# Kernel tuning notes

Hardware: AMD Instinct MI355X
Metric: run time of the kernel (lower is better)

## Reference

```python
import jax, jax.numpy as jnp
import numpy as np
import math

F_DIM = 512
N_HEADS = 8
HEAD_DIM = F_DIM // N_HEADS
IMG = 16            # image_size
L = IMG ** 3        # voxel sequence length = 4096
PATCH = 196         # patch_number (ViT 14x14)
VIT_RES = 14
RES = 224           # VIEW_IMAGE_RES
SKETCH_DIM = 768
SIGMA = 1.5         # fixed kernel_size (torch draws randomly when None)
GN_GROUPS = 32


def position_encoding(d_model, length):
    pe = np.zeros((length, d_model), dtype=np.float32)
    position = np.arange(length, dtype=np.float32)[:, None]
    div_term = np.exp(np.arange(0, d_model, 2, dtype=np.float32) * -(math.log(10000.0) / d_model))
    pe[:, 0::2] = np.sin(position * div_term)
    pe[:, 1::2] = np.cos(position * div_term)
    return jnp.asarray(pe)


def get_voxel_coordinates(resolution, size=1.0):
    # centers of a resolution^3 grid spanning [-size/2, size/2]
    idx = np.arange(resolution, dtype=np.float32)
    g = np.stack(np.meshgrid(idx, idx, idx, indexing='ij'), -1).reshape(-1, 3)
    return (g + 0.5) / resolution * size - size / 2.0


VOXEL_PE = position_encoding(F_DIM, L)          # (L, F)
COND_PE = position_encoding(F_DIM, PATCH)       # (S, F)
VOXEL_PTS = jnp.asarray(get_voxel_coordinates(IMG))  # (L, 3)
_vg = np.arange(VIT_RES, dtype=np.float32)
VIT_PIXELS = jnp.asarray(np.stack(np.meshgrid(_vg, _vg, indexing='ij'), -1).reshape(PATCH, 2))  # (S, 2)


def setup_inputs() -> dict:
    key = jax.random.key(0)
    ks = jax.random.split(key, 12)
    B = 8
    s = 0.02
    return {
        'x': jax.random.normal(ks[0], (B, F_DIM, IMG, IMG, IMG), jnp.float32),
        'sketch_feature': jax.random.normal(ks[1], (B, PATCH, SKETCH_DIM), jnp.float32),
        'projection_matrix': jax.random.normal(ks[2], (B, 1, 3, 3), jnp.float32),
        'gn_scale': jnp.ones((F_DIM,), jnp.float32),
        'gn_bias': jnp.zeros((F_DIM,), jnp.float32),
        'conv_w': jax.random.normal(ks[3], (F_DIM, F_DIM, 3, 3, 3), jnp.float32) * s,
        'conv_b': jnp.zeros((F_DIM,), jnp.float32),
        'k_w': jax.random.normal(ks[4], (F_DIM, SKETCH_DIM), jnp.float32) * s,
        'k_b': jnp.zeros((F_DIM,), jnp.float32),
        'v_w': jax.random.normal(ks[5], (F_DIM, SKETCH_DIM), jnp.float32) * s,
        'v_b': jnp.zeros((F_DIM,), jnp.float32),
        'in_proj_w': jax.random.normal(ks[6], (3 * F_DIM, F_DIM), jnp.float32) * s,
        'in_proj_b': jnp.zeros((3 * F_DIM,), jnp.float32),
        'out_w': jax.random.normal(ks[7], (F_DIM, F_DIM), jnp.float32) * s,
        'out_b': jnp.zeros((F_DIM,), jnp.float32),
    }


def _group_norm(x, scale, bias, groups=GN_GROUPS, eps=1e-5):
    B, C = x.shape[0], x.shape[1]
    xr = x.reshape(B, groups, C // groups, -1)
    m = xr.mean(axis=(2, 3), keepdims=True)
    v = xr.var(axis=(2, 3), keepdims=True)
    xn = ((xr - m) / jnp.sqrt(v + eps)).reshape(x.shape)
    shp = (1, C) + (1,) * (x.ndim - 2)
    return xn * scale.reshape(shp) + bias.reshape(shp)


def _attn_mask(projection_matrix):
    # project voxel centers, clamp to pixel grid, threshold cdist to vit patch centers
    P = projection_matrix[:, 0]                                  # (B,3,3)
    pc = jnp.einsum('bij,nj->bni', P, VOXEL_PTS)                 # (B,L,3)
    pixels = pc[..., 0:2] / pc[..., 2:3]
    pixels = jnp.clip(jnp.round(pixels), 0.0, RES - 1.0)         # clamp_pixel
    x_idx = (2.0 * pixels[..., 1:2] + 1.0) / RES * VIT_RES / 2.0
    y_idx = (2.0 * (RES - 1.0 - pixels[..., 0:1]) + 1.0) / RES * VIT_RES / 2.0
    ps = jnp.concatenate([x_idx, y_idx], -1) - 0.5               # (B,L,2)
    dist = jnp.linalg.norm(ps[:, :, None, :] - VIT_PIXELS[None, None], axis=-1)  # (B,L,S)
    return jnp.abs(dist) > (SIGMA - 1e-6)                        # True = masked out


def _forward(x, sketch_feature, projection_matrix, gn_scale, gn_bias, conv_w, conv_b,
             k_w, k_b, v_w, v_b, in_proj_w, in_proj_b, out_w, out_b):
    B = x.shape[0]
    # q path: GroupNorm -> SiLU -> Conv3d(3, pad 1)
    h = jax.nn.silu(_group_norm(x, gn_scale, gn_bias))
    h = jax.lax.conv_general_dilated(h, conv_w, window_strides=(1, 1, 1),
                                     padding=[(1, 1)] * 3,
                                     dimension_numbers=('NCDHW', 'OIDHW', 'NCDHW'))
    h = h + conv_b.reshape(1, F_DIM, 1, 1, 1)
    q = h.reshape(B, F_DIM, L).transpose(0, 2, 1) + VOXEL_PE[None]        # (B,L,F)

    mask = _attn_mask(projection_matrix)                                   # (B,L,S)

    k = sketch_feature @ k_w.T + k_b + COND_PE[None]                       # (B,S,F)
    v = sketch_feature @ v_w.T + v_b + COND_PE[None]

    # nn.MultiheadAttention (eval: no dropout)
    wq, wk, wv = jnp.split(in_proj_w, 3, axis=0)
    bq, bk, bv = jnp.split(in_proj_b, 3, axis=0)
    qh = (q @ wq.T + bq).reshape(B, L, N_HEADS, HEAD_DIM).transpose(0, 2, 1, 3)
    kh = (k @ wk.T + bk).reshape(B, PATCH, N_HEADS, HEAD_DIM).transpose(0, 2, 1, 3)
    vh = (v @ wv.T + bv).reshape(B, PATCH, N_HEADS, HEAD_DIM).transpose(0, 2, 1, 3)

    scores = jnp.einsum('bhld,bhsd->bhls', qh, kh) / math.sqrt(HEAD_DIM)   # (B,H,L,S)
    scores = jnp.where(mask[:, None], -jnp.inf, scores)                    # mask shared over heads
    attn = jax.nn.softmax(scores, axis=-1)
    o = jnp.einsum('bhls,bhsd->bhld', attn, vh)
    o = o.transpose(0, 2, 1, 3).reshape(B, L, F_DIM)
    o = o @ out_w.T + out_b                                                # (B,L,F)
    return o.transpose(0, 2, 1).reshape(B, F_DIM, IMG, IMG, IMG)


def reference(x, sketch_feature, projection_matrix, gn_scale, gn_bias, conv_w, conv_b,
              k_w, k_b, v_w, v_b, in_proj_w, in_proj_b, out_w, out_b):
    return _forward(x, sketch_feature, projection_matrix, gn_scale, gn_bias, conv_w, conv_b,
                    k_w, k_b, v_w, v_b, in_proj_w, in_proj_b, out_w, out_b)
```

## Files before the change

kernel.cpp:

```cpp
#include <hip/hip_runtime.h>

#define DEV static __device__ __forceinline__

typedef unsigned short u16;
typedef unsigned int u32;
typedef unsigned long long u64;
typedef float f32x4 __attribute__((ext_vector_type(4)));
typedef short bfrag __attribute__((ext_vector_type(8)));

#define FD 512
#define LV 4096
#define PV 5832

DEV float b2f(u16 u){ union{ u32 i; float f; } x; x.i = ((u32)u)<<16; return x.f; }
DEV u16 f2b(float f){ union{ float f; u32 i; } x; x.f = f; u32 r = x.i; r += 0x7fffu + ((r>>16)&1u); return (u16)(r>>16); }

DEV void g2l(const void* g, void* s){
  __builtin_amdgcn_global_load_lds((const __attribute__((address_space(1))) void*)g,
                                   (__attribute__((address_space(3))) void*)s, 16, 0, 0);
}

static const size_t o_wt  = 0;
static const size_t o_wq  = 14155776;
static const size_t o_ow  = 14680064;
static const size_t o_vpe = 15204352;
static const size_t o_cpe = 23592960;
static const size_t o_gn  = 23994368;
static const size_t o_mask= 23996416;
static const size_t o_khb = 25044992;
static const size_t o_vhb = 26748928;
static const size_t o_hp  = 36841472;
static const size_t o_qb  = 84617216;
static const size_t o_qh  = 118171648;
static const size_t o_skb = o_qh;
static const size_t o_kwb = o_qh + 2555904;
static const size_t o_vwb = o_qh + 3342336;
static const size_t o_wkb = o_qh + 4128768;
static const size_t o_wvb = o_qh + 4653056;
static const size_t o_ktb = o_qh + 5177344;
static const size_t o_vtb = o_qh + 6881280;

__global__ __launch_bounds__(256) void prep_all(const float* __restrict__ convw,
    const float* __restrict__ ipw, const float* __restrict__ ow,
    const float* __restrict__ sketch, const float* __restrict__ kw, const float* __restrict__ vw,
    u16* __restrict__ wt, u16* __restrict__ Wq, u16* __restrict__ Ow, u16* __restrict__ Skb,
    u16* __restrict__ Kwb, u16* __restrict__ Vwb, u16* __restrict__ Wkb, u16* __restrict__ Wvb){
  __shared__ float raw[6912];
  int blk = blockIdx.x, t = threadIdx.x;
  if (blk < 1024){
    size_t base = (size_t)blk*6912;
    #pragma unroll
    for (int j=0;j<27;j++) raw[j*256 + t] = convw[base + j*256 + t];
    __syncthreads();
    int rowb = blk*256;
    #pragma unroll
    for (int k=0;k<27;k++) wt[(size_t)k*262144 + rowb + t] = f2b(raw[t*27 + k]);
  } else if (blk < 2048){ int i=(blk-1024)*256+t;  Wq[i]  = f2b(ipw[i]); }
  else if (blk < 3072){   int i=(blk-2048)*256+t;  Ow[i]  = f2b(ow[i]); }
  else if (blk < 7776){   int i=(blk-3072)*256+t;  if (i<1204224) Skb[i] = f2b(sketch[i]); }
  else if (blk < 9312){   int i=(blk-7776)*256+t;  Kwb[i] = f2b(kw[i]); }
  else if (blk < 10848){  int i=(blk-9312)*256+t;  Vwb[i] = f2b(vw[i]); }
  else if (blk < 11872){  int i=(blk-10848)*256+t; Wkb[i] = f2b(ipw[262144+i]); }
  else {                  int i=(blk-11872)*256+t; Wvb[i] = f2b(ipw[524288+i]); }
}

__global__ __launch_bounds__(256) void geom_prep(float* __restrict__ vpe, float* __restrict__ cpe,
    const float* __restrict__ proj, u64* __restrict__ maskb){
  int blk = blockIdx.x, t = threadIdx.x;
  if (blk < 4292){
    float* pe = (blk < 4096) ? vpe : cpe;
    int l = (blk < 4096) ? blk : blk - 4096;
    const float fac = -0.017988946039015984f;
    float dt = expf((float)(2*t) * fac);
    float ang = (float)l * dt;
    pe[(size_t)l*FD + 2*t]     = sinf(ang);
    pe[(size_t)l*FD + 2*t + 1] = cosf(ang);
    return;
  }
  int idx = (blk-4292)*256 + t;
  int b = idx >> 12, v = idx & 4095;
  float P[9];
  #pragma unroll
  for (int j=0;j<9;j++) P[j] = proj[b*9 + j];
  int zi=v>>8, yi=(v>>4)&15, xi=v&15;
  float pt0 = ((float)zi + 0.5f)/16.0f - 0.5f;
  float pt1 = ((float)yi + 0.5f)/16.0f - 0.5f;
  float pt2 = ((float)xi + 0.5f)/16.0f - 0.5f;
  float pc0 = __fadd_rn(__fadd_rn(__fmul_rn(P[0],pt0), __fmul_rn(P[1],pt1)), __fmul_rn(P[2],pt2));
  float pc1 = __fadd_rn(__fadd_rn(__fmul_rn(P[3],pt0), __fmul_rn(P[4],pt1)), __fmul_rn(P[5],pt2));
  float pc2 = __fadd_rn(__fadd_rn(__fmul_rn(P[6],pt0), __fmul_rn(P[7],pt1)), __fmul_rn(P[8],pt2));
  float r0 = __fdiv_rn(pc0, pc2);
  float r1 = __fdiv_rn(pc1, pc2);
  float px0 = fminf(fmaxf(rintf(r0), 0.f), 223.f);
  float px1 = fminf(fmaxf(rintf(r1), 0.f), 223.f);
  float x_idx = __fmul_rn(__fdiv_rn(__fadd_rn(__fmul_rn(2.f,px1),1.f), 224.f), 14.f) * 0.5f;
  float y_idx = __fmul_rn(__fdiv_rn(__fadd_rn(__fmul_rn(2.f,__fadd_rn(223.f,-px0)),1.f), 224.f), 14.f) * 0.5f;
  float ps0 = __fadd_rn(x_idx, -0.5f);
  float ps1 = __fadd_rn(y_idx, -0.5f);
  const float TH = 1.4999990463256836f;
  u64 abits[4] = {0,0,0,0};
  #pragma unroll 1
  for (int s=0;s<196;s++){
    int si = s/14, sj = s - si*14;
    float d0 = __fadd_rn(ps0, -(float)si);
    float d1 = __fadd_rn(ps1, -(float)sj);
    float dist = sqrtf(__fadd_rn(__fmul_rn(d0,d0), __fmul_rn(d1,d1)));
    if (!(fabsf(dist) > TH)) abits[s>>6] |= (1ull << (s&63));
  }
  int cube = (zi>>2)*16 + (yi>>2)*4 + (xi>>2);
  int cl = cube*64 + (zi&3)*16 + (yi&3)*4 + (xi&3);
  u64* out = maskb + ((size_t)b*4096 + cl)*4;
  out[0]=abits[0]; out[1]=abits[1]; out[2]=abits[2]; out[3]=abits[3];
}

__global__ __launch_bounds__(256) void gn_stats(const float* __restrict__ x, float* __restrict__ stats){
  int bg = blockIdx.x;
  const float* base = x + (size_t)bg*65536;
  float s=0.f, q=0.f;
  for (int i=threadIdx.x;i<65536;i+=256){ float v = base[i]; s+=v; q+=v*v; }
  #pragma unroll
  for (int off=32; off>0; off>>=1){ s += __shfl_xor(s,off); q += __shfl_xor(q,off); }
  __shared__ float red[8];
  int w = threadIdx.x>>6;
  if ((threadIdx.x&63)==0){ red[w*2]=s; red[w*2+1]=q; }
  __syncthreads();
  if (threadIdx.x==0){
    float S=red[0]+red[2]+red[4]+red[6];
    float Q=red[1]+red[3]+red[5]+red[7];
    float m = S*(1.f/65536.f);
    float var = Q*(1.f/65536.f) - m*m;
    stats[bg] = m;
    stats[256+bg] = rsqrtf(var + 1e-5f);
  }
}

__global__ __launch_bounds__(256) void gn_apply_t(const float* __restrict__ x,
    const float* __restrict__ stats, const float* __restrict__ sc, const float* __restrict__ bi,
    u16* __restrict__ hp){
  __shared__ u16 tile[64][66];
  int vb = blockIdx.x, cb = blockIdx.y, b = blockIdx.z;
  int t = threadIdx.x, w = t>>6, l = t&63;
  int v0 = vb*64, c0 = cb*64;
  const float* xb = x + (size_t)b*FD*LV;
  #pragma unroll
  for (int p=0;p<16;p++){
    int cc = p*4 + w;
    int c = c0 + cc;
    float val = xb[(size_t)c*LV + v0 + l];
    int g = c>>4;
    float m = stats[b*32+g];
    float r = stats[256 + b*32+g];
    float xn = (val - m)*r*sc[c] + bi[c];
    tile[cc][l] = f2b(xn / (1.f + expf(-xn)));
  }
  __syncthreads();
  u16* hpb = hp + (size_t)b*PV*FD;
  #pragma unroll
  for (int p=0;p<16;p++){
    int vv = p*4 + w;
    int v = v0 + vv;
    int z = v>>8, y = (v>>4)&15, xx = v&15;
    size_t hrow = ((size_t)(z+1)*324 + (size_t)(y+1)*18 + (xx+1))*FD;
    hpb[hrow + c0 + l] = tile[l][vv];
  }
}

__global__ __launch_bounds__(256,4) void conv_mfma(const u16* __restrict__ hp,
    const u16* __restrict__ wt, const float* __restrict__ cbias,
    const float* __restrict__ vpe, u16* __restrict__ qb){
  __shared__ __align__(16) u16 Al[8192];
  __shared__ __align__(16) u16 Wl[8192];
  int tid = threadIdx.x;
  int w = tid>>6, l = tid&63;
  int v0 = blockIdx.x*128, n0 = blockIdx.y*128, b = blockIdx.z;
  int swz = ((l&7) ^ ((l>>3)&7))*8;
  size_t abase[4], wbase[4];
  #pragma unroll
  for (int j=0;j<4;j++){
    int r = w*32 + j*8 + (l>>3);
    int v = v0 + r;
    int z = v>>8, yy=(v>>4)&15, xx=v&15;
    abase[j] = ((size_t)b*PV + (size_t)(z*324 + yy*18 + xx))*FD + swz;
    wbase[j] = (size_t)(n0 + r)*FD + swz;
  }
  f32x4 zero4 = {0.f,0.f,0.f,0.f};
  f32x4 acc[4][4];
  #pragma unroll
  for (int i=0;i<4;i++)
    #pragma unroll
    for (int j=0;j<4;j++) acc[i][j] = zero4;
  int wr = (w>>1)*64, wc = (w&1)*64;
  for (int kk=0; kk<216; ++kk){
    int off = kk>>3;
    int ks  = (kk&7)<<6;
    int dz = off/9; int rem = off - dz*9; int dy = rem/3; int dx = rem - dy*3;
    size_t adelta = (size_t)(dz*324 + dy*18 + dx)*FD + ks;
    size_t wdelta = (size_t)off*262144 + ks;
    #pragma unroll
    for (int j=0;j<4;j++){
      g2l(hp + abase[j] + adelta, Al + (w*32 + j*8)*64);
      g2l(wt + wbase[j] + wdelta, Wl + (w*32 + j*8)*64);
    }
    __syncthreads();
    #pragma unroll
    for (int ks2=0; ks2<2; ++ks2){
      bfrag af[4], wf[4];
      #pragma unroll
      for (int i=0;i<4;i++){
        int ra = wr + i*16 + (l&15);
        af[i] = *(const bfrag*)(Al + ra*64 + (((ks2<<2) + (l>>4)) ^ (l&7))*8);
        int rb = wc + i*16 + (l&15);
        wf[i] = *(const bfrag*)(Wl + rb*64 + (((ks2<<2) + (l>>4)) ^ (l&7))*8);
      }
      #pragma unroll
      for (int i=0;i<4;i++)
        #pragma unroll
        for (int j=0;j<4;j++)
          acc[i][j] = __builtin_amdgcn_mfma_f32_16x16x32_bf16(af[i], wf[j], acc[i][j], 0,0,0);
    }
    __syncthreads();
  }
  #pragma unroll
  for (int i=0;i<4;i++)
    #pragma unroll
    for (int j=0;j<4;j++)
      #pragma unroll
      for (int rg=0;rg<4;rg++){
        int row = wr + i*16 + ((l>>4)<<2) + rg;
        int col = wc + j*16 + (l&15);
        int v = v0 + row, n = n0 + col;
        float cv = acc[i][j][rg] + cbias[n] + vpe[(size_t)v*FD + n];
        qb[((size_t)b*LV + v)*FD + n] = f2b(cv);
      }
}

template<bool TRANS>
__global__ __launch_bounds__(256,4) void gemm_mfma(const u16* __restrict__ A, const u16* __restrict__ W,
    const float* __restrict__ bias, void* __restrict__ Cout){
  __shared__ __align__(16) u16 Al[8192];
  __shared__ __align__(16) u16 Wl[8192];
  int tid = threadIdx.x;
  int w = tid>>6, l = tid&63;
  int m0 = blockIdx.x*128, n0 = blockIdx.y*128, b = blockIdx.z;
  int swz = ((l&7) ^ ((l>>3)&7))*8;
  size_t abase[4], wbase[4];
  #pragma unroll
  for (int j=0;j<4;j++){
    int r = w*32 + j*8 + (l>>3);
    abase[j] = ((size_t)b*LV + m0 + r)*FD + swz;
    wbase[j] = (size_t)(n0 + r)*FD + swz;
  }
  f32x4 zero4 = {0.f,0.f,0.f,0.f};
  f32x4 acc[4][4];
  #pragma unroll
  for (int i=0;i<4;i++)
    #pragma unroll
    for (int j=0;j<4;j++) acc[i][j] = zero4;
  int wr = (w>>1)*64, wc = (w&1)*64;
  for (int kk=0; kk<8; ++kk){
    size_t kd = (size_t)kk*64;
    #pragma unroll
    for (int j=0;j<4;j++){
      g2l(A + abase[j] + kd, Al + (w*32 + j*8)*64);
      g2l(W + wbase[j] + kd, Wl + (w*32 + j*8)*64);
    }
    __syncthreads();
    #pragma unroll
    for (int ks2=0; ks2<2; ++ks2){
      bfrag af[4], wf[4];
      #pragma unroll
      for (int i=0;i<4;i++){
        int ra = wr + i*16 + (l&15);
        af[i] = *(const bfrag*)(Al + ra*64 + (((ks2<<2) + (l>>4)) ^ (l&7))*8);
        int rb = wc + i*16 + (l&15);
        wf[i] = *(const bfrag*)(Wl + rb*64 + (((ks2<<2) + (l>>4)) ^ (l&7))*8);
      }
      #pragma unroll
      for (int i=0;i<4;i++)
        #pragma unroll
        for (int j=0;j<4;j++)
          acc[i][j] = __builtin_amdgcn_mfma_f32_16x16x32_bf16(af[i], wf[j], acc[i][j], 0,0,0);
    }
    __syncthreads();
  }
  #pragma unroll
  for (int i=0;i<4;i++)
    #pragma unroll
    for (int j=0;j<4;j++){
      if constexpr (TRANS){
        int row = m0 + wr + i*16 + ((l>>4)<<2);
        int col = n0 + wc + j*16 + (l&15);
        float bv = bias[col];
        float4 val = { acc[i][j][0]+bv, acc[i][j][1]+bv, acc[i][j][2]+bv, acc[i][j][3]+bv };
        *(float4*)&(((float*)Cout)[((size_t)b*FD + col)*LV + row]) = val;
      } else {
        #pragma unroll
        for (int rg=0;rg<4;rg++){
          int row = m0 + wr + i*16 + ((l>>4)<<2) + rg;
          int col = n0 + wc + j*16 + (l&15);
          ((u16*)Cout)[((size_t)b*LV + row)*FD + col] = f2b(acc[i][j][rg] + bias[col]);
        }
      }
    }
}

template<bool ADDPE>
__global__ __launch_bounds__(256,2) void gemm_kv(const u16* __restrict__ A0, const u16* __restrict__ A1,
    const u16* __restrict__ W0, const u16* __restrict__ W1,
    const float* __restrict__ b0, const float* __restrict__ b1,
    const float* __restrict__ pe, u16* __restrict__ C0, u16* __restrict__ C1, int K){
  const u16* A = blockIdx.z ? A1 : A0;
  const u16* W = blockIdx.z ? W1 : W0;
  const float* bias = blockIdx.z ? b1 : b0;
  u16* Cout = blockIdx.z ? C1 : C0;
  __shared__ __align__(16) u16 Al[4096];
  __shared__ __align__(16) u16 Wl[4096];
  int tid = threadIdx.x;
  int w = tid>>6, l = tid&63;
  int m0 = blockIdx.x*128, n0 = blockIdx.y*128;
  int sw_src = (((l&3) ^ ((l>>3)&3)))*8;
  int sw_rd  = (((l>>4) ^ ((l>>1)&3)))*8;
  size_t abase[2], wbase[2];
  #pragma unroll
  for (int j=0;j<2;j++){
    int r = (w*2+j)*16 + (l>>2);
    abase[j] = (size_t)(m0 + r)*K + sw_src;
    wbase[j] = (size_t)(n0 + r)*K + sw_src;
  }
  f32x4 zero4 = {0.f,0.f,0.f,0.f};
  f32x4 acc[4][4];
  #pragma unroll
  for (int i=0;i<4;i++)
    #pragma unroll
    for (int j=0;j<4;j++) acc[i][j] = zero4;
  int wr = (w>>1)*64, wc = (w&1)*64;
  for (int k0=0; k0<K; k0+=32){
    #pragma unroll
    for (int j=0;j<2;j++){
      g2l(A + abase[j] + k0, Al + (w*2+j)*512);
      g2l(W + wbase[j] + k0, Wl + (w*2+j)*512);
    }
    __syncthreads();
    bfrag af[4], wf[4];
    #pragma unroll
    for (int i=0;i<4;i++){
      int r  = wr + i*16 + (l&15);
      af[i] = *(const bfrag*)(Al + r*32 + sw_rd);
      int cn = wc + i*16 + (l&15);
      wf[i] = *(const bfrag*)(Wl + cn*32 + sw_rd);
    }
    #pragma unroll
    for (int i=0;i<4;i++)
      #pragma unroll
      for (int j=0;j<4;j++)
        acc[i][j] = __builtin_amdgcn_mfma_f32_16x16x32_bf16(af[i], wf[j], acc[i][j], 0,0,0);
    __syncthreads();
  }
  #pragma unroll
  for (int i=0;i<4;i++)
    #pragma unroll
    for (int j=0;j<4;j++)
      #pragma unroll
      for (int rg=0;rg<4;rg++){
        int row = m0 + wr + i*16 + ((l>>4)<<2) + rg;
        int col = n0 + wc + j*16 + (l&15);
        float cv = acc[i][j][rg] + bias[col];
        if constexpr (ADDPE) cv += pe[(size_t)(row % 196)*FD + col];
        Cout[(size_t)row*FD + col] = f2b(cv);
      }
}

__global__ __launch_bounds__(256) void attn_lit(const u16* __restrict__ qh,
    const u16* __restrict__ khb, const u16* __restrict__ vhb,
    const u64* __restrict__ maskb, u16* __restrict__ obuf){
  __shared__ u16 ot[4][64][66];
  int t = threadIdx.x, w = t>>6, l = t&63;
  int h = blockIdx.y, b = blockIdx.z;
  int cube = blockIdx.x*4 + w;
  int cz = cube>>4, cy = (cube>>2)&3, cx = cube&3;
  int v = (cz*4 + (l>>4))*256 + (cy*4 + ((l>>2)&3))*16 + (cx*4 + (l&3));
  int cl = cube*64 + l;
  const u64* mrow = maskb + ((size_t)b*LV + cl)*4;
  u64 abits[4] = {mrow[0], mrow[1], mrow[2], mrow[3]};

  float qr[64];
  {
    const uint4* qp = (const uint4*)(qh + ((size_t)b*LV + v)*FD + h*64);
    #pragma unroll
    for (int c=0;c<8;c++){
      uint4 u = qp[c];
      qr[c*8+0]=b2f((u16)(u.x&0xffffu)); qr[c*8+1]=b2f((u16)(u.x>>16));
      qr[c*8+2]=b2f((u16)(u.y&0xffffu)); qr[c*8+3]=b2f((u16)(u.y>>16));
      qr[c*8+4]=b2f((u16)(u.z&0xffffu)); qr[c*8+5]=b2f((u16)(u.z>>16));
      qr[c*8+6]=b2f((u16)(u.w&0xffffu)); qr[c*8+7]=b2f((u16)(u.w>>16));
    }
  }
  const u16* kb = khb + (size_t)(b*196)*FD + h*64;
  const u16* vb = vhb + (size_t)(b*196)*FD + h*64;
  float o[64];
  #pragma unroll
  for (int d=0;d<64;d++) o[d]=0.f;
  float ssum = 0.f;
  for (int s=0;s<196;s++){
    if (!((abits[s>>6] >> (s&63)) & 1ull)) continue;
    const uint4* kr = (const uint4*)(kb + (size_t)s*FD);
    float dot = 0.f;
    #pragma unroll
    for (int c=0;c<8;c++){
      uint4 u = kr[c];
      dot += qr[c*8+0]*b2f((u16)(u.x&0xffffu)) + qr[c*8+1]*b2f((u16)(u.x>>16))
           + qr[c*8+2]*b2f((u16)(u.y&0xffffu)) + qr[c*8+3]*b2f((u16)(u.y>>16))
           + qr[c*8+4]*b2f((u16)(u.z&0xffffu)) + qr[c*8+5]*b2f((u16)(u.z>>16))
           + qr[c*8+6]*b2f((u16)(u.w&0xffffu)) + qr[c*8+7]*b2f((u16)(u.w>>16));
    }
    float e = expf(dot*0.125f);
    ssum += e;
    const uint4* vr = (const uint4*)(vb + (size_t)s*FD);
    #pragma unroll
    for (int c=0;c<8;c++){
      uint4 u = vr[c];
      o[c*8+0] += e*b2f((u16)(u.x&0xffffu)); o[c*8+1] += e*b2f((u16)(u.x>>16));
      o[c*8+2] += e*b2f((u16)(u.y&0xffffu)); o[c*8+3] += e*b2f((u16)(u.y>>16));
      o[c*8+4] += e*b2f((u16)(u.z&0xffffu)); o[c*8+5] += e*b2f((u16)(u.z>>16));
      o[c*8+6] += e*b2f((u16)(u.w&0xffffu)); o[c*8+7] += e*b2f((u16)(u.w>>16));
    }
  }
  float inv = (ssum > 0.f) ? 1.f/ssum : 0.f;
  u32* orow = (u32*)&ot[w][l][0];
  #pragma unroll
  for (int c=0;c<32;c++){
    u32 lo = f2b(o[c*2]*inv);
    u32 hi = f2b(o[c*2+1]*inv);
    orow[c] = lo | (hi<<16);
  }
  #pragma unroll 4
  for (int s=0;s<64;s++){
    int vs = (cz*4 + (s>>4))*256 + (cy*4 + ((s>>2)&3))*16 + (cx*4 + (s&3));
    obuf[((size_t)b*LV + vs)*FD + h*64 + l] = ot[w][s][l];
  }
}

extern "C" void kernel_launch(void* const* d_in, const int* in_sizes, int n_in,
                              void* d_out, int out_size, void* d_ws, size_t ws_size,
                              hipStream_t stream) {
  (void)in_sizes; (void)n_in; (void)out_size; (void)ws_size;
  const float* x_in  = (const float*)d_in[0];
  const float* sketch= (const float*)d_in[1];
  const float* projm = (const float*)d_in[2];
  const float* gnsc  = (const float*)d_in[3];
  const float* gnbi  = (const float*)d_in[4];
  const float* convw = (const float*)d_in[5];
  const float* convb = (const float*)d_in[6];
  const float* kw_in = (const float*)d_in[7];
  const float* kb_in = (const float*)d_in[8];
  const float* vw_in = (const float*)d_in[9];
  const float* vb_in = (const float*)d_in[10];
  const float* ipw   = (const float*)d_in[11];
  const float* ipb   = (const float*)d_in[12];
  const float* ow_in = (const float*)d_in[13];
  const float* ob_in = (const float*)d_in[14];
  char* ws = (char*)d_ws;
  u16*   wt   = (u16*)(ws + o_wt);
  u16*   Wq   = (u16*)(ws + o_wq);
  u16*   Ow   = (u16*)(ws + o_ow);
  float* vpe  = (float*)(ws + o_vpe);
  float* cpe  = (float*)(ws + o_cpe);
  float* stats= (float*)(ws + o_gn);
  u64*   maskb= (u64*)(ws + o_mask);
  u16*   khb  = (u16*)(ws + o_khb);
  u16*   vhb  = (u16*)(ws + o_vhb);
  u16*   hp   = (u16*)(ws + o_hp);
  u16*   qb   = (u16*)(ws + o_qb);
  u16*   qhb  = (u16*)(ws + o_qh);
  u16*   Skb  = (u16*)(ws + o_skb);
  u16*   Kwb  = (u16*)(ws + o_kwb);
  u16*   Vwb  = (u16*)(ws + o_vwb);
  u16*   Wkb  = (u16*)(ws + o_wkb);
  u16*   Wvb  = (u16*)(ws + o_wvb);
  u16*   ktb  = (u16*)(ws + o_ktb);
  u16*   vtb  = (u16*)(ws + o_vtb);
  u16*   obuf = qb;

  hipMemsetAsync(hp, 0, 47775744, stream);
  hipMemsetAsync((char*)Skb + 2408448, 0, 147456, stream);
  prep_all<<<12896,256,0,stream>>>(convw, ipw, ow_in, sketch, kw_in, vw_in,
                                   wt, Wq, Ow, Skb, Kwb, Vwb, Wkb, Wvb);
  geom_prep<<<4420,256,0,stream>>>(vpe, cpe, projm, maskb);
  gn_stats<<<256,256,0,stream>>>(x_in, stats);
  gemm_kv<true ><<<dim3(13,4,2),256,0,stream>>>(Skb, Skb, Kwb, Vwb, kb_in, vb_in, cpe, ktb, vtb, 768);
  gemm_kv<false><<<dim3(13,4,2),256,0,stream>>>(ktb, vtb, Wkb, Wvb, ipb+512, ipb+1024, nullptr, khb, vhb, 512);

  gn_apply_t<<<dim3(64,8,8),256,0,stream>>>(x_in, stats, gnsc, gnbi, hp);
  conv_mfma<<<dim3(32,4,8),256,0,stream>>>(hp, wt, convb, vpe, qb);
  gemm_mfma<false><<<dim3(32,4,8),256,0,stream>>>(qb, Wq, ipb, qhb);
  attn_lit<<<dim3(16,8,8),256,0,stream>>>(qhb, khb, vhb, maskb, obuf);
  gemm_mfma<true ><<<dim3(32,4,8),256,0,stream>>>(obuf, Ow, ob_in, d_out);
}
```

Measured before the change: 737.4 us.

## Double-buffer conv LDS tiles to overlap global loads with MFMA

The implicit-GEMM conv kernel now keeps two LDS buffers for the A and W tiles. It prefetches the next k-slice with global_load_lds while running MFMAs on the current one, and uses explicit vmcnt waits with raw s_barrier. The goal is to hide global memory latency that was previously exposed on every one of the 216 k-iterations. In exchange, LDS per block doubles and launch bounds drop from 4 to 2 blocks per CU, which can lower occupancy. The correctness of the vmcnt/barrier ordering also depends on the compiler not reordering the waits.

```diff
diff --git a/kernel.cpp b/kernel.cpp
--- a/kernel.cpp
+++ b/kernel.cpp
@@ -165,16 +165,17 @@
   }
 }
 
-__global__ __launch_bounds__(256,4) void conv_mfma(const u16* __restrict__ hp,
+__global__ __launch_bounds__(256,2) void conv_mfma(const u16* __restrict__ hp,
     const u16* __restrict__ wt, const float* __restrict__ cbias,
     const float* __restrict__ vpe, u16* __restrict__ qb){
-  __shared__ __align__(16) u16 Al[8192];
-  __shared__ __align__(16) u16 Wl[8192];
+  __shared__ __align__(16) u16 Al[16384];
+  __shared__ __align__(16) u16 Wl[16384];
   int tid = threadIdx.x;
   int w = tid>>6, l = tid&63;
   int v0 = blockIdx.x*128, n0 = blockIdx.y*128, b = blockIdx.z;
   int swz = ((l&7) ^ ((l>>3)&7))*8;
   size_t abase[4], wbase[4];
+  int lrow[4];
   #pragma unroll
   for (int j=0;j<4;j++){
     int r = w*32 + j*8 + (l>>3);
@@ -182,6 +183,7 @@
     int z = v>>8, yy=(v>>4)&15, xx=v&15;
     abase[j] = ((size_t)b*PV + (size_t)(z*324 + yy*18 + xx))*FD + swz;
     wbase[j] = (size_t)(n0 + r)*FD + swz;
+    lrow[j] = (w*32 + j*8)*64;
   }
   f32x4 zero4 = {0.f,0.f,0.f,0.f};
   f32x4 acc[4][4];
@@ -190,27 +192,44 @@
     #pragma unroll
     for (int j=0;j<4;j++) acc[i][j] = zero4;
   int wr = (w>>1)*64, wc = (w&1)*64;
+
+  {
+    #pragma unroll
+    for (int j=0;j<4;j++){
+      g2l(hp + abase[j], Al + lrow[j]);
+      g2l(wt + wbase[j], Wl + lrow[j]);
+    }
+  }
   for (int kk=0; kk<216; ++kk){
-    int off = kk>>3;
-    int ks  = (kk&7)<<6;
-    int dz = off/9; int rem = off - dz*9; int dy = rem/3; int dx = rem - dy*3;
-    size_t adelta = (size_t)(dz*324 + dy*18 + dx)*FD + ks;
-    size_t wdelta = (size_t)off*262144 + ks;
-    #pragma unroll
-    for (int j=0;j<4;j++){
-      g2l(hp + abase[j] + adelta, Al + (w*32 + j*8)*64);
-      g2l(wt + wbase[j] + wdelta, Wl + (w*32 + j*8)*64);
-    }
-    __syncthreads();
+    int cur = kk & 1;
+    int nbuf = (cur^1)*8192;
+    if (kk < 215){
+      int kn = kk + 1;
+      int off = kn>>3;
+      int ks  = (kn&7)<<6;
+      int dz = off/9; int rem = off - dz*9; int dy = rem/3; int dx = rem - dy*3;
+      size_t adelta = (size_t)(dz*324 + dy*18 + dx)*FD + ks;
+      size_t wdelta = (size_t)off*262144 + ks;
+      #pragma unroll
+      for (int j=0;j<4;j++){
+        g2l(hp + abase[j] + adelta, Al + nbuf + lrow[j]);
+        g2l(wt + wbase[j] + wdelta, Wl + nbuf + lrow[j]);
+      }
+      asm volatile("s_waitcnt vmcnt(8)" ::: "memory");
+    } else {
+      asm volatile("s_waitcnt vmcnt(0)" ::: "memory");
+    }
+    __builtin_amdgcn_s_barrier();
+    int cb0 = cur*8192;
     #pragma unroll
     for (int ks2=0; ks2<2; ++ks2){
       bfrag af[4], wf[4];
       #pragma unroll
       for (int i=0;i<4;i++){
         int ra = wr + i*16 + (l&15);
-        af[i] = *(const bfrag*)(Al + ra*64 + (((ks2<<2) + (l>>4)) ^ (l&7))*8);
+        af[i] = *(const bfrag*)(Al + cb0 + ra*64 + (((ks2<<2) + (l>>4)) ^ (l&7))*8);
         int rb = wc + i*16 + (l&15);
-        wf[i] = *(const bfrag*)(Wl + rb*64 + (((ks2<<2) + (l>>4)) ^ (l&7))*8);
+        wf[i] = *(const bfrag*)(Wl + cb0 + rb*64 + (((ks2<<2) + (l>>4)) ^ (l&7))*8);
       }
       #pragma unroll
       for (int i=0;i<4;i++)
@@ -218,7 +237,8 @@
         for (int j=0;j<4;j++)
           acc[i][j] = __builtin_amdgcn_mfma_f32_16x16x32_bf16(af[i], wf[j], acc[i][j], 0,0,0);
     }
-    __syncthreads();
+    __builtin_amdgcn_sched_barrier(0);
+    __builtin_amdgcn_s_barrier();
   }
   #pragma unroll
   for (int i=0;i<4;i++)
```

Measured after the change: 835.6 us. 13.3% more time.

## Merge independent setup, KV GEMM, GroupNorm and conv launches into fewer kernels

Applied to the files above, without the earlier changes.

Combines the weight prep, geometry/mask prep and GroupNorm stats into one launch. The first KV GEMM is now fused with the GroupNorm apply, and the second KV GEMM with the conv, by dispatching on block index. The aim is to cut launch overhead and let small independent work fill the GPU alongside larger kernels. In exchange, the merged kernels carry the larger shared-memory footprint and register pressure of their heaviest branch, and the fused conv kernel now runs KV GEMM blocks under a 4-waves launch bound.

```diff
diff --git a/kernel.cpp b/kernel.cpp
--- a/kernel.cpp
+++ b/kernel.cpp
@@ -40,107 +40,188 @@
 static const size_t o_ktb = o_qh + 5177344;
 static const size_t o_vtb = o_qh + 6881280;
 
-__global__ __launch_bounds__(256) void prep_all(const float* __restrict__ convw,
+__global__ __launch_bounds__(256) void setup1(const float* __restrict__ convw,
     const float* __restrict__ ipw, const float* __restrict__ ow,
     const float* __restrict__ sketch, const float* __restrict__ kw, const float* __restrict__ vw,
     u16* __restrict__ wt, u16* __restrict__ Wq, u16* __restrict__ Ow, u16* __restrict__ Skb,
-    u16* __restrict__ Kwb, u16* __restrict__ Vwb, u16* __restrict__ Wkb, u16* __restrict__ Wvb){
+    u16* __restrict__ Kwb, u16* __restrict__ Vwb, u16* __restrict__ Wkb, u16* __restrict__ Wvb,
+    float* __restrict__ vpe, float* __restrict__ cpe,
+    const float* __restrict__ proj, u64* __restrict__ maskb,
+    const float* __restrict__ x, float* __restrict__ stats){
   __shared__ float raw[6912];
+  __shared__ float red[8];
   int blk = blockIdx.x, t = threadIdx.x;
-  if (blk < 1024){
-    size_t base = (size_t)blk*6912;
-    #pragma unroll
-    for (int j=0;j<27;j++) raw[j*256 + t] = convw[base + j*256 + t];
-    __syncthreads();
-    int rowb = blk*256;
-    #pragma unroll
-    for (int k=0;k<27;k++) wt[(size_t)k*262144 + rowb + t] = f2b(raw[t*27 + k]);
-  } else if (blk < 2048){ int i=(blk-1024)*256+t;  Wq[i]  = f2b(ipw[i]); }
-  else if (blk < 3072){   int i=(blk-2048)*256+t;  Ow[i]  = f2b(ow[i]); }
-  else if (blk < 7776){   int i=(blk-3072)*256+t;  if (i<1204224) Skb[i] = f2b(sketch[i]); }
-  else if (blk < 9312){   int i=(blk-7776)*256+t;  Kwb[i] = f2b(kw[i]); }
-  else if (blk < 10848){  int i=(blk-9312)*256+t;  Vwb[i] = f2b(vw[i]); }
-  else if (blk < 11872){  int i=(blk-10848)*256+t; Wkb[i] = f2b(ipw[262144+i]); }
-  else {                  int i=(blk-11872)*256+t; Wvb[i] = f2b(ipw[524288+i]); }
-}
-
-__global__ __launch_bounds__(256) void geom_prep(float* __restrict__ vpe, float* __restrict__ cpe,
-    const float* __restrict__ proj, u64* __restrict__ maskb){
-  int blk = blockIdx.x, t = threadIdx.x;
-  if (blk < 4292){
-    float* pe = (blk < 4096) ? vpe : cpe;
-    int l = (blk < 4096) ? blk : blk - 4096;
-    const float fac = -0.017988946039015984f;
-    float dt = expf((float)(2*t) * fac);
-    float ang = (float)l * dt;
-    pe[(size_t)l*FD + 2*t]     = sinf(ang);
-    pe[(size_t)l*FD + 2*t + 1] = cosf(ang);
+  if (blk < 12896){
+    if (blk < 1024){
+      size_t base = (size_t)blk*6912;
+      #pragma unroll
+      for (int j=0;j<27;j++) raw[j*256 + t] = convw[base + j*256 + t];
+      __syncthreads();
+      int rowb = blk*256;
+      #pragma unroll
+      for (int k=0;k<27;k++) wt[(size_t)k*262144 + rowb + t] = f2b(raw[t*27 + k]);
+    } else if (blk < 2048){ int i=(blk-1024)*256+t;  Wq[i]  = f2b(ipw[i]); }
+    else if (blk < 3072){   int i=(blk-2048)*256+t;  Ow[i]  = f2b(ow[i]); }
+    else if (blk < 7776){   int i=(blk-3072)*256+t;  if (i<1204224) Skb[i] = f2b(sketch[i]); }
+    else if (blk < 9312){   int i=(blk-7776)*256+t;  Kwb[i] = f2b(kw[i]); }
+    else if (blk < 10848){  int i=(blk-9312)*256+t;  Vwb[i] = f2b(vw[i]); }
+    else if (blk < 11872){  int i=(blk-10848)*256+t; Wkb[i] = f2b(ipw[262144+i]); }
+    else {                  int i=(blk-11872)*256+t; Wvb[i] = f2b(ipw[524288+i]); }
     return;
   }
-  int idx = (blk-4292)*256 + t;
-  int b = idx >> 12, v = idx & 4095;
-  float P[9];
-  #pragma unroll
-  for (int j=0;j<9;j++) P[j] = proj[b*9 + j];
-  int zi=v>>8, yi=(v>>4)&15, xi=v&15;
-  float pt0 = ((float)zi + 0.5f)/16.0f - 0.5f;
-  float pt1 = ((float)yi + 0.5f)/16.0f - 0.5f;
-  float pt2 = ((float)xi + 0.5f)/16.0f - 0.5f;
-  float pc0 = __fadd_rn(__fadd_rn(__fmul_rn(P[0],pt0), __fmul_rn(P[1],pt1)), __fmul_rn(P[2],pt2));
-  float pc1 = __fadd_rn(__fadd_rn(__fmul_rn(P[3],pt0), __fmul_rn(P[4],pt1)), __fmul_rn(P[5],pt2));
-  float pc2 = __fadd_rn(__fadd_rn(__fmul_rn(P[6],pt0), __fmul_rn(P[7],pt1)), __fmul_rn(P[8],pt2));
-  float r0 = __fdiv_rn(pc0, pc2);
-  float r1 = __fdiv_rn(pc1, pc2);
-  float px0 = fminf(fmaxf(rintf(r0), 0.f), 223.f);
-  float px1 = fminf(fmaxf(rintf(r1), 0.f), 223.f);
-  float x_idx = __fmul_rn(__fdiv_rn(__fadd_rn(__fmul_rn(2.f,px1),1.f), 224.f), 14.f) * 0.5f;
-  float y_idx = __fmul_rn(__fdiv_rn(__fadd_rn(__fmul_rn(2.f,__fadd_rn(223.f,-px0)),1.f), 224.f), 14.f) * 0.5f;
-  float ps0 = __fadd_rn(x_idx, -0.5f);
-  float ps1 = __fadd_rn(y_idx, -0.5f);
-  const float TH = 1.4999990463256836f;
-  u64 abits[4] = {0,0,0,0};
-  #pragma unroll 1
-  for (int s=0;s<196;s++){
-    int si = s/14, sj = s - si*14;
-    float d0 = __fadd_rn(ps0, -(float)si);
-    float d1 = __fadd_rn(ps1, -(float)sj);
-    float dist = sqrtf(__fadd_rn(__fmul_rn(d0,d0), __fmul_rn(d1,d1)));
-    if (!(fabsf(dist) > TH)) abits[s>>6] |= (1ull << (s&63));
-  }
-  int cube = (zi>>2)*16 + (yi>>2)*4 + (xi>>2);
-  int cl = cube*64 + (zi&3)*16 + (yi&3)*4 + (xi&3);
-  u64* out = maskb + ((size_t)b*4096 + cl)*4;
-  out[0]=abits[0]; out[1]=abits[1]; out[2]=abits[2]; out[3]=abits[3];
-}
-
-__global__ __launch_bounds__(256) void gn_stats(const float* __restrict__ x, float* __restrict__ stats){
-  int bg = blockIdx.x;
-  const float* base = x + (size_t)bg*65536;
-  float s=0.f, q=0.f;
-  for (int i=threadIdx.x;i<65536;i+=256){ float v = base[i]; s+=v; q+=v*v; }
-  #pragma unroll
-  for (int off=32; off>0; off>>=1){ s += __shfl_xor(s,off); q += __shfl_xor(q,off); }
-  __shared__ float red[8];
-  int w = threadIdx.x>>6;
-  if ((threadIdx.x&63)==0){ red[w*2]=s; red[w*2+1]=q; }
-  __syncthreads();
-  if (threadIdx.x==0){
-    float S=red[0]+red[2]+red[4]+red[6];
-    float Q=red[1]+red[3]+red[5]+red[7];
-    float m = S*(1.f/65536.f);
-    float var = Q*(1.f/65536.f) - m*m;
-    stats[bg] = m;
-    stats[256+bg] = rsqrtf(var + 1e-5f);
-  }
-}
-
-__global__ __launch_bounds__(256) void gn_apply_t(const float* __restrict__ x,
-    const float* __restrict__ stats, const float* __restrict__ sc, const float* __restrict__ bi,
-    u16* __restrict__ hp){
+  if (blk < 17316){
+    int gb = blk - 12896;
+    if (gb < 4292){
+      float* pe = (gb < 4096) ? vpe : cpe;
+      int l = (gb < 4096) ? gb : gb - 4096;
+      const float fac = -0.017988946039015984f;
+      float dt = expf((float)(2*t) * fac);
+      float ang = (float)l * dt;
+      pe[(size_t)l*FD + 2*t]     = sinf(ang);
+      pe[(size_t)l*FD + 2*t + 1] = cosf(ang);
+      return;
+    }
+    int idx = (gb-4292)*256 + t;
+    int b = idx >> 12, v = idx & 4095;
+    float P[9];
+    #pragma unroll
+    for (int j=0;j<9;j++) P[j] = proj[b*9 + j];
+    int zi=v>>8, yi=(v>>4)&15, xi=v&15;
+    float pt0 = ((float)zi + 0.5f)/16.0f - 0.5f;
+    float pt1 = ((float)yi + 0.5f)/16.0f - 0.5f;
+    float pt2 = ((float)xi + 0.5f)/16.0f - 0.5f;
+    float pc0 = __fadd_rn(__fadd_rn(__fmul_rn(P[0],pt0), __fmul_rn(P[1],pt1)), __fmul_rn(P[2],pt2));
+    float pc1 = __fadd_rn(__fadd_rn(__fmul_rn(P[3],pt0), __fmul_rn(P[4],pt1)), __fmul_rn(P[5],pt2));
+    float pc2 = __fadd_rn(__fadd_rn(__fmul_rn(P[6],pt0), __fmul_rn(P[7],pt1)), __fmul_rn(P[8],pt2));
+    float r0 = __fdiv_rn(pc0, pc2);
+    float r1 = __fdiv_rn(pc1, pc2);
+    float px0 = fminf(fmaxf(rintf(r0), 0.f), 223.f);
+    float px1 = fminf(fmaxf(rintf(r1), 0.f), 223.f);
+    float x_idx = __fmul_rn(__fdiv_rn(__fadd_rn(__fmul_rn(2.f,px1),1.f), 224.f), 14.f) * 0.5f;
+    float y_idx = __fmul_rn(__fdiv_rn(__fadd_rn(__fmul_rn(2.f,__fadd_rn(223.f,-px0)),1.f), 224.f), 14.f) * 0.5f;
+    float ps0 = __fadd_rn(x_idx, -0.5f);
+    float ps1 = __fadd_rn(y_idx, -0.5f);
+    const float TH = 1.4999990463256836f;
+    u64 abits[4] = {0,0,0,0};
+    #pragma unroll 1
+    for (int s=0;s<196;s++){
+      int si = s/14, sj = s - si*14;
+      float d0 = __fadd_rn(ps0, -(float)si);
+      float d1 = __fadd_rn(ps1, -(float)sj);
+      float dist = sqrtf(__fadd_rn(__fmul_rn(d0,d0), __fmul_rn(d1,d1)));
+      if (!(fabsf(dist) > TH)) abits[s>>6] |= (1ull << (s&63));
+    }
+    int cube = (zi>>2)*16 + (yi>>2)*4 + (xi>>2);
+    int cl = cube*64 + (zi&3)*16 + (yi&3)*4 + (xi&3);
+    u64* out = maskb + ((size_t)b*4096 + cl)*4;
+    out[0]=abits[0]; out[1]=abits[1]; out[2]=abits[2]; out[3]=abits[3];
+    return;
+  }
+  {
+    int bg = blk - 17316;
+    const float* base = x + (size_t)bg*65536;
+    float s=0.f, q=0.f;
+    for (int i=t;i<65536;i+=256){ float v = base[i]; s+=v; q+=v*v; }
+    #pragma unroll
+    for (int off=32; off>0; off>>=1){ s += __shfl_xor(s,off); q += __shfl_xor(q,off); }
+    int w = t>>6;
+    if ((t&63)==0){ red[w*2]=s; red[w*2+1]=q; }
+    __syncthreads();
+    if (t==0){
+      float S=red[0]+red[2]+red[4]+red[6];
+      float Q=red[1]+red[3]+red[5]+red[7];
+      float m = S*(1.f/65536.f);
+      float var = Q*(1.f/65536.f) - m*m;
+      stats[bg] = m;
+      stats[256+bg] = rsqrtf(var + 1e-5f);
+    }
+  }
+}
+
+template<bool ADDPE>
+DEV void kv_body(int bx, int by, int bz,
+    const u16* __restrict__ A0, const u16* __restrict__ A1,
+    const u16* __restrict__ W0, const u16* __restrict__ W1,
+    const float* __restrict__ b0, const float* __restrict__ b1,
+    const float* __restrict__ pe, u16* __restrict__ C0, u16* __restrict__ C1, int K,
+    u16* Al, u16* Wl){
+  const u16* A = bz ? A1 : A0;
+  const u16* W = bz ? W1 : W0;
+  const float* bias = bz ? b1 : b0;
+  u16* Cout = bz ? C1 : C0;
+  int tid = threadIdx.x;
+  int w = tid>>6, l = tid&63;
+  int m0 = bx*128, n0 = by*128;
+  int sw_src = (((l&3) ^ ((l>>3)&3)))*8;
+  int sw_rd  = (((l>>4) ^ ((l>>1)&3)))*8;
+  size_t abase[2], wbase[2];
+  #pragma unroll
+  for (int j=0;j<2;j++){
+    int r = (w*2+j)*16 + (l>>2);
+    abase[j] = (size_t)(m0 + r)*K + sw_src;
+    wbase[j] = (size_t)(n0 + r)*K + sw_src;
+  }
+  f32x4 zero4 = {0.f,0.f,0.f,0.f};
+  f32x4 acc[4][4];
+  #pragma unroll
+  for (int i=0;i<4;i++)
+    #pragma unroll
+    for (int j=0;j<4;j++) acc[i][j] = zero4;
+  int wr = (w>>1)*64, wc = (w&1)*64;
+  for (int k0=0; k0<K; k0+=32){
+    #pragma unroll
+    for (int j=0;j<2;j++){
+      g2l(A + abase[j] + k0, Al + (w*2+j)*512);
+      g2l(W + wbase[j] + k0, Wl + (w*2+j)*512);
+    }
+    __syncthreads();
+    bfrag af[4], wf[4];
+    #pragma unroll
+    for (int i=0;i<4;i++){
+      int r  = wr + i*16 + (l&15);
+      af[i] = *(const bfrag*)(Al + r*32 + sw_rd);
+      int cn = wc + i*16 + (l&15);
+      wf[i] = *(const bfrag*)(Wl + cn*32 + sw_rd);
+    }
+    #pragma unroll
+    for (int i=0;i<4;i++)
+      #pragma unroll
+      for (int j=0;j<4;j++)
+        acc[i][j] = __builtin_amdgcn_mfma_f32_16x16x32_bf16(af[i], wf[j], acc[i][j], 0,0,0);
+    __syncthreads();
+  }
+  #pragma unroll
+  for (int i=0;i<4;i++)
+    #pragma unroll
+    for (int j=0;j<4;j++)
+      #pragma unroll
+      for (int rg=0;rg<4;rg++){
+        int row = m0 + wr + i*16 + ((l>>4)<<2) + rg;
+        int col = n0 + wc + j*16 + (l&15);
+        float cv = acc[i][j][rg] + bias[col];
+        if constexpr (ADDPE) cv += pe[(size_t)(row % 196)*FD + col];
+        Cout[(size_t)row*FD + col] = f2b(cv);
+      }
+}
+
+__global__ __launch_bounds__(256,4) void fuse2(
+    const u16* __restrict__ Skb, const u16* __restrict__ Kwb, const u16* __restrict__ Vwb,
+    const float* __restrict__ kb, const float* __restrict__ vb, const float* __restrict__ cpe,
+    u16* __restrict__ ktb, u16* __restrict__ vtb,
+    const float* __restrict__ x, const float* __restrict__ stats,
+    const float* __restrict__ sc, const float* __restrict__ bi, u16* __restrict__ hp){
+  __shared__ __align__(16) u16 Al[4096];
+  __shared__ __align__(16) u16 Wl[4096];
   __shared__ u16 tile[64][66];
-  int vb = blockIdx.x, cb = blockIdx.y, b = blockIdx.z;
+  int blk = blockIdx.x;
+  if (blk < 104){
+    kv_body<true>(blk%13, (blk/13)%4, blk/52, Skb, Skb, Kwb, Vwb, kb, vb, cpe, ktb, vtb, 768, Al, Wl);
+    return;
+  }
+  int i = blk - 104;
+  int vb2 = i & 63, cb = (i>>6)&7, b = i>>9;
   int t = threadIdx.x, w = t>>6, l = t&63;
-  int v0 = vb*64, c0 = cb*64;
+  int v0 = vb2*64, c0 = cb*64;
   const float* xb = x + (size_t)b*FD*LV;
   #pragma unroll
   for (int p=0;p<16;p++){
@@ -165,14 +246,23 @@
   }
 }
 
-__global__ __launch_bounds__(256,4) void conv_mfma(const u16* __restrict__ hp,
+__global__ __launch_bounds__(256,4) void fuse3(const u16* __restrict__ hp,
     const u16* __restrict__ wt, const float* __restrict__ cbias,
-    const float* __restrict__ vpe, u16* __restrict__ qb){
+    const float* __restrict__ vpe, u16* __restrict__ qb,
+    const u16* __restrict__ ktb, const u16* __restrict__ vtb,
+    const u16* __restrict__ Wkb, const u16* __restrict__ Wvb,
+    const float* __restrict__ ipb, u16* __restrict__ khb, u16* __restrict__ vhb){
   __shared__ __align__(16) u16 Al[8192];
   __shared__ __align__(16) u16 Wl[8192];
+  int blk = blockIdx.x;
+  if (blk >= 1024){
+    int i = blk - 1024;
+    kv_body<false>(i%13, (i/13)%4, i/52, ktb, vtb, Wkb, Wvb, ipb+512, ipb+1024, nullptr, khb, vhb, 512, Al, Wl);
+    return;
+  }
   int tid = threadIdx.x;
   int w = tid>>6, l = tid&63;
-  int v0 = blockIdx.x*128, n0 = blockIdx.y*128, b = blockIdx.z;
+  int v0 = (blk & 31)*128, n0 = ((blk>>5)&3)*128, b = blk>>7;
   int swz = ((l&7) ^ ((l>>3)&7))*8;
   size_t abase[4], wbase[4];
   #pragma unroll
@@ -302,72 +392,6 @@
         }
       }
     }
-}
-
-template<bool ADDPE>
-__global__ __launch_bounds__(256,2) void gemm_kv(const u16* __restrict__ A0, const u16* __restrict__ A1,
-    const u16* __restrict__ W0, const u16* __restrict__ W1,
-    const float* __restrict__ b0, const float* __restrict__ b1,
-    const float* __restrict__ pe, u16* __restrict__ C0, u16* __restrict__ C1, int K){
-  const u16* A = blockIdx.z ? A1 : A0;
-  const u16* W = blockIdx.z ? W1 : W0;
-  const float* bias = blockIdx.z ? b1 : b0;
-  u16* Cout = blockIdx.z ? C1 : C0;
-  __shared__ __align__(16) u16 Al[4096];
-  __shared__ __align__(16) u16 Wl[4096];
-  int tid = threadIdx.x;
-  int w = tid>>6, l = tid&63;
-  int m0 = blockIdx.x*128, n0 = blockIdx.y*128;
-  int sw_src = (((l&3) ^ ((l>>3)&3)))*8;
-  int sw_rd  = (((l>>4) ^ ((l>>1)&3)))*8;
-  size_t abase[2], wbase[2];
-  #pragma unroll
-  for (int j=0;j<2;j++){
-    int r = (w*2+j)*16 + (l>>2);
-    abase[j] = (size_t)(m0 + r)*K + sw_src;
-    wbase[j] = (size_t)(n0 + r)*K + sw_src;
-  }
-  f32x4 zero4 = {0.f,0.f,0.f,0.f};
-  f32x4 acc[4][4];
-  #pragma unroll
-  for (int i=0;i<4;i++)
-    #pragma unroll
-    for (int j=0;j<4;j++) acc[i][j] = zero4;
-  int wr = (w>>1)*64, wc = (w&1)*64;
-  for (int k0=0; k0<K; k0+=32){
-    #pragma unroll
-    for (int j=0;j<2;j++){
-      g2l(A + abase[j] + k0, Al + (w*2+j)*512);
-      g2l(W + wbase[j] + k0, Wl + (w*2+j)*512);
-    }
-    __syncthreads();
-    bfrag af[4], wf[4];
-    #pragma unroll
-    for (int i=0;i<4;i++){
-      int r  = wr + i*16 + (l&15);
-      af[i] = *(const bfrag*)(Al + r*32 + sw_rd);
-      int cn = wc + i*16 + (l&15);
-      wf[i] = *(const bfrag*)(Wl + cn*32 + sw_rd);
-    }
-    #pragma unroll
-    for (int i=0;i<4;i++)
-      #pragma unroll
-      for (int j=0;j<4;j++)
-        acc[i][j] = __builtin_amdgcn_mfma_f32_16x16x32_bf16(af[i], wf[j], acc[i][j], 0,0,0);
-    __syncthreads();
-  }
-  #pragma unroll
-  for (int i=0;i<4;i++)
-    #pragma unroll
-    for (int j=0;j<4;j++)
-      #pragma unroll
-      for (int rg=0;rg<4;rg++){
-        int row = m0 + wr + i*16 + ((l>>4)<<2) + rg;
-        int col = n0 + wc + j*16 + (l&15);
-        float cv = acc[i][j][rg] + bias[col];
-        if constexpr (ADDPE) cv += pe[(size_t)(row % 196)*FD + col];
-        Cout[(size_t)row*FD + col] = f2b(cv);
-      }
 }
 
 __global__ __launch_bounds__(256) void attn_lit(const u16* __restrict__ qh,
@@ -483,15 +507,13 @@
 
   hipMemsetAsync(hp, 0, 47775744, stream);
   hipMemsetAsync((char*)Skb + 2408448, 0, 147456, stream);
-  prep_all<<<12896,256,0,stream>>>(convw, ipw, ow_in, sketch, kw_in, vw_in,
-                                   wt, Wq, Ow, Skb, Kwb, Vwb, Wkb, Wvb);
-  geom_prep<<<4420,256,0,stream>>>(vpe, cpe, projm, maskb);
-  gn_stats<<<256,256,0,stream>>>(x_in, stats);
-  gemm_kv<true ><<<dim3(13,4,2),256,0,stream>>>(Skb, Skb, Kwb, Vwb, kb_in, vb_in, cpe, ktb, vtb, 768);
-  gemm_kv<false><<<dim3(13,4,2),256,0,stream>>>(ktb, vtb, Wkb, Wvb, ipb+512, ipb+1024, nullptr, khb, vhb, 512);
-
-  gn_apply_t<<<dim3(64,8,8),256,0,stream>>>(x_in, stats, gnsc, gnbi, hp);
-  conv_mfma<<<dim3(32,4,8),256,0,stream>>>(hp, wt, convb, vpe, qb);
+  setup1<<<17572,256,0,stream>>>(convw, ipw, ow_in, sketch, kw_in, vw_in,
+                                 wt, Wq, Ow, Skb, Kwb, Vwb, Wkb, Wvb,
+                                 vpe, cpe, projm, maskb, x_in, stats);
+  fuse2<<<4200,256,0,stream>>>(Skb, Kwb, Vwb, kb_in, vb_in, cpe, ktb, vtb,
+                               x_in, stats, gnsc, gnbi, hp);
+  fuse3<<<1128,256,0,stream>>>(hp, wt, convb, vpe, qb,
+                               ktb, vtb, Wkb, Wvb, ipb, khb, vhb);
   gemm_mfma<false><<<dim3(32,4,8),256,0,stream>>>(qb, Wq, ipb, qhb);
   attn_lit<<<dim3(16,8,8),256,0,stream>>>(qhb, khb, vhb, maskb, obuf);
   gemm_mfma<true ><<<dim3(32,4,8),256,0,stream>>>(obuf, Ow, ob_in, d_out);
```

Result: faster. 687.5 us (-6.8%).
